# Performance work log

Measured on AMD Instinct MI355X. Metric: run time of the kernel, lower is better.

The kernel has to match this reference:

```python
import jax, jax.numpy as jnp
import numpy as np

N_, CIN, H_, W_ = 2, 128, 240, 320
C_, HEADS, WS, DEPTH, HID, DOUT, NQ = 128, 4, 7, 4, 512, 256, 128

def _ln(x, g, b, eps=1e-5):
    mu = x.mean(-1, keepdims=True)
    var = ((x - mu) ** 2).mean(-1, keepdims=True)
    return (x - mu) / jnp.sqrt(var + eps) * g + b

def setup_inputs() -> dict:
    key = jax.random.key(0)
    ks = jax.random.split(key, 16)
    s = 0.02
    d = {}
    d['x'] = jax.random.normal(ks[0], (N_, CIN, H_, W_), jnp.float32)
    d['conv_w'] = jax.random.normal(ks[1], (C_, CIN), jnp.float32) * s
    d['conv_b'] = jnp.zeros((C_,), jnp.float32)
    d['n1_g'] = jnp.ones((DEPTH, C_), jnp.float32)
    d['n1_b'] = jnp.zeros((DEPTH, C_), jnp.float32)
    d['qkv_w'] = jax.random.normal(ks[2], (DEPTH, 3 * C_, C_), jnp.float32) * s
    d['qkv_b'] = jnp.zeros((DEPTH, 3 * C_), jnp.float32)
    d['proj_w'] = jax.random.normal(ks[3], (DEPTH, C_, C_), jnp.float32) * s
    d['proj_b'] = jnp.zeros((DEPTH, C_), jnp.float32)
    d['n2_g'] = jnp.ones((DEPTH, C_), jnp.float32)
    d['n2_b'] = jnp.zeros((DEPTH, C_), jnp.float32)
    d['fc1_w'] = jax.random.normal(ks[4], (DEPTH, HID, C_), jnp.float32) * s
    d['fc1_b'] = jnp.zeros((DEPTH, HID), jnp.float32)
    d['fc2_w'] = jax.random.normal(ks[5], (DEPTH, C_, HID), jnp.float32) * s
    d['fc2_b'] = jnp.zeros((DEPTH, C_), jnp.float32)
    d['r1_w'] = jax.random.normal(ks[6], (256, C_), jnp.float32) * s
    d['r1_b'] = jnp.zeros((256,), jnp.float32)
    d['r2_w'] = jax.random.normal(ks[7], (256, 256), jnp.float32) * s
    d['r2_b'] = jnp.zeros((256,), jnp.float32)
    d['r3_w'] = jax.random.normal(ks[8], (DOUT, 256), jnp.float32) * s
    d['r3_b'] = jnp.zeros((DOUT,), jnp.float32)
    return d

def _block(t, H, W, n1_g, n1_b, qkv_w, qkv_b, proj_w, proj_b, n2_g, n2_b, fc1_w, fc1_b, fc2_w, fc2_b):
    N, L, C = t.shape
    hd = C // HEADS
    scale = hd ** -0.5
    shortcut = t
    h = _ln(t, n1_g, n1_b).reshape(N, H, W, C)
    pad_h = (-H) % WS
    pad_w = (-W) % WS
    h = jnp.pad(h, ((0, 0), (0, pad_h), (0, pad_w), (0, 0)))
    Hp, Wp = H + pad_h, W + pad_w
    # partition into (num_windows*N, ws*ws, C)
    h = h.reshape(N, Hp // WS, WS, Wp // WS, WS, C).transpose(0, 1, 3, 2, 4, 5).reshape(-1, WS * WS, C)
    B_ = h.shape[0]
    qkv = (h @ qkv_w.T + qkv_b).reshape(B_, WS * WS, 3, HEADS, hd).transpose(2, 0, 3, 1, 4)
    q, k, v = qkv[0], qkv[1], qkv[2]
    attn = jax.nn.softmax(jnp.einsum('bhqd,bhkd->bhqk', q, k) * scale, axis=-1)
    o = jnp.einsum('bhqk,bhkd->bhqd', attn, v).transpose(0, 2, 1, 3).reshape(B_, WS * WS, C)
    o = o @ proj_w.T + proj_b
    # reverse window partition
    o = o.reshape(N, Hp // WS, Wp // WS, WS, WS, C).transpose(0, 1, 3, 2, 4, 5).reshape(N, Hp, Wp, C)[:, :H, :W, :].reshape(N, H * W, C)
    t = shortcut + o
    h2 = _ln(t, n2_g, n2_b)
    m = jax.nn.gelu(h2 @ fc1_w.T + fc1_b, approximate=False) @ fc2_w.T + fc2_b
    return t + m

def reference(x, conv_w, conv_b, n1_g, n1_b, qkv_w, qkv_b, proj_w, proj_b, n2_g, n2_b, fc1_w, fc1_b, fc2_w, fc2_b, r1_w, r1_b, r2_w, r2_b, r3_w, r3_b):
    N, Cin, H, W = x.shape
    xp = jnp.einsum('nchw,ec->nehw', x, conv_w) + conv_b[None, :, None, None]  # (N,C,H,W)
    tokens = xp.reshape(N, C_, H * W).transpose(0, 2, 1)  # (N,HW,C)
    for i in range(DEPTH):
        tokens = _block(tokens, H, W, n1_g[i], n1_b[i], qkv_w[i], qkv_b[i], proj_w[i], proj_b[i], n2_g[i], n2_b[i], fc1_w[i], fc1_b[i], fc2_w[i], fc2_b[i])
    head = tokens.mean(axis=1)  # (N,C)
    queries = tokens[:, :NQ, :]  # (N,NQ,C)
    maps = jnp.einsum('nchw,nqc->nqhw', xp, queries)  # PixelWiseDotProduct
    y = jax.nn.leaky_relu(head @ r1_w.T + r1_b, 0.01)
    y = jax.nn.leaky_relu(y @ r2_w.T + r2_b, 0.01)
    y = y @ r3_w.T + r3_b
    y = jax.nn.relu(y) + 0.1  # norm == 'linear'
    y = y / y.sum(axis=1, keepdims=True)
    return (y, maps)
```

## Files before the change

kernel.cpp:

```cpp
#include <hip/hip_runtime.h>
#include <hip/hip_bf16.h>

typedef __hip_bfloat16 bf16;

static constexpr int Nn = 2, CIN = 128, Hh = 240, Ww = 320, HW = 76800;
static constexpr int Cc = 128, HID = 512, DOUT = 256, WSQ = 49;
static constexpr int NWH = 35, NWW = 46, WPN = NWH * NWW;
static constexpr int NWIN = Nn * WPN;
static constexpr float SCALE = 0.17677669529663687f;

typedef __attribute__((ext_vector_type(8))) short s8;
typedef __attribute__((ext_vector_type(4))) short s4;
typedef __attribute__((ext_vector_type(2))) short s2;
typedef __attribute__((ext_vector_type(4))) float f4;

__device__ __forceinline__ short f2bf(float x) {
  union { bf16 b; short s; } u; u.b = __float2bfloat16(x); return u.s;
}

#define MFMA(a, b, c) __builtin_amdgcn_mfma_f32_16x16x32_bf16((a), (b), (c), 0, 0, 0)

__global__ __launch_bounds__(256) void cast_bf16(const float* __restrict__ src,
                                                 short* __restrict__ dst, int n) {
  const int i = (blockIdx.x * 256 + threadIdx.x) * 4;
  if (i < n) {
    const float4 v = *(const float4*)(src + i);
    s4 o; o[0] = f2bf(v.x); o[1] = f2bf(v.y); o[2] = f2bf(v.z); o[3] = f2bf(v.w);
    *(s4*)(dst + i) = o;
  }
}

__global__ void init_head(float* headbuf) {
  if (threadIdx.x < 256) headbuf[threadIdx.x] = 0.f;
}

__global__ __launch_bounds__(256) void transp_w(const float* __restrict__ conv_w,
                                                float* __restrict__ wT) {
  const int idx = blockIdx.x * 256 + threadIdx.x;
  const int c = idx >> 7, e = idx & 127;
  wT[c * 128 + e] = conv_w[e * 128 + c];
}

__global__ __launch_bounds__(256) void conv_kernel(
    const float* __restrict__ x, const float* __restrict__ wT, const float* __restrict__ conv_b,
    float* __restrict__ tok) {
  __shared__ float wlds[64 * 128];
  const int tid = threadIdx.x;
  const int lane = tid & 63, w = tid >> 6;
  const int n = blockIdx.y;
  const int hw0 = blockIdx.x * 128;
  const int hwi = 2 * lane;
  const int e0 = 32 * w;
  const float* xn = x + (size_t)n * CIN * HW + hw0 + hwi;
  float acc[2][32];
#pragma unroll
  for (int jj = 0; jj < 8; jj++) {
    const float4 b4 = *(const float4*)(conv_b + e0 + jj * 4);
    acc[0][jj*4+0] = b4.x; acc[1][jj*4+0] = b4.x;
    acc[0][jj*4+1] = b4.y; acc[1][jj*4+1] = b4.y;
    acc[0][jj*4+2] = b4.z; acc[1][jj*4+2] = b4.z;
    acc[0][jj*4+3] = b4.w; acc[1][jj*4+3] = b4.w;
  }
  for (int ch = 0; ch < 2; ch++) {
    if (ch) __syncthreads();
    for (int idx = tid * 4; idx < 8192; idx += 1024)
      *(float4*)(wlds + idx) = *(const float4*)(wT + ch * 8192 + idx);
    __syncthreads();
    const float* xc = xn + (size_t)(64 * ch) * HW;
    float2 xv = *(const float2*)(xc);
    for (int cc = 0; cc < 64; cc++) {
      const float2 nxt = *(const float2*)(xc + (size_t)(cc < 63 ? cc + 1 : 63) * HW);
      const float* wl = wlds + cc * 128 + e0;
#pragma unroll
      for (int jj = 0; jj < 8; jj++) {
        const float4 w4 = *(const float4*)(wl + jj * 4);
        acc[0][jj*4+0] = fmaf(w4.x, xv.x, acc[0][jj*4+0]); acc[1][jj*4+0] = fmaf(w4.x, xv.y, acc[1][jj*4+0]);
        acc[0][jj*4+1] = fmaf(w4.y, xv.x, acc[0][jj*4+1]); acc[1][jj*4+1] = fmaf(w4.y, xv.y, acc[1][jj*4+1]);
        acc[0][jj*4+2] = fmaf(w4.z, xv.x, acc[0][jj*4+2]); acc[1][jj*4+2] = fmaf(w4.z, xv.y, acc[1][jj*4+2]);
        acc[0][jj*4+3] = fmaf(w4.w, xv.x, acc[0][jj*4+3]); acc[1][jj*4+3] = fmaf(w4.w, xv.y, acc[1][jj*4+3]);
      }
      xv = nxt;
    }
  }
  float* tb0 = tok + ((size_t)n * HW + hw0 + hwi) * Cc + e0;
  float* tb1 = tb0 + Cc;
#pragma unroll
  for (int jj = 0; jj < 8; jj++) {
    *(float4*)(tb0 + jj * 4) = make_float4(acc[0][jj*4], acc[0][jj*4+1], acc[0][jj*4+2], acc[0][jj*4+3]);
    *(float4*)(tb1 + jj * 4) = make_float4(acc[1][jj*4], acc[1][jj*4+1], acc[1][jj*4+2], acc[1][jj*4+3]);
  }
}

__global__ __launch_bounds__(256, 2) void attn_kernel(
    float* __restrict__ tok,
    const float* __restrict__ n1_g, const float* __restrict__ n1_b,
    const short* __restrict__ wqkv, const float* __restrict__ qkv_b,
    const short* __restrict__ wproj, const float* __restrict__ proj_b,
    int layer) {
  __shared__ __align__(16) short ms[27136];
  short* xwv = ms + 17920;

  const int tid = threadIdx.x;
  const int w = tid >> 6, lane = tid & 63;
  const int lq = lane >> 4, li = lane & 15;
  const int wi = blockIdx.x;
  const int n = wi / WPN;
  const int r0 = wi % WPN;
  const int wh = r0 / NWW, ww = r0 % NWW;

  const short* wqkv_l = wqkv + (size_t)layer * 384 * 128;
  const short* wproj_l = wproj + (size_t)layer * 128 * 128;

  for (int ti = w; ti < WSQ; ti += 4) {
    const int hh = wh * 7 + ti / 7, wv = ww * 7 + ti % 7;
    const bool valid = (hh < Hh) && (wv < Ww);
    float2 v = make_float2(0.f, 0.f);
    if (valid) v = *(const float2*)(tok + ((size_t)n * HW + hh * Ww + wv) * Cc + 2 * lane);
    float s = v.x + v.y, q = v.x * v.x + v.y * v.y;
#pragma unroll
    for (int m = 1; m < 64; m <<= 1) { s += __shfl_xor(s, m); q += __shfl_xor(q, m); }
    const float mean = s * (1.f / 128.f);
    const float rstd = rsqrtf(fmaxf(q * (1.f / 128.f) - mean * mean, 0.f) + 1e-5f);
    const int c = 2 * lane;
    float o0 = 0.f, o1 = 0.f;
    if (valid) {
      o0 = (v.x - mean) * rstd * n1_g[layer * Cc + c]     + n1_b[layer * Cc + c];
      o1 = (v.y - mean) * rstd * n1_g[layer * Cc + c + 1] + n1_b[layer * Cc + c + 1];
    }
    s2 pk; pk[0] = f2bf(o0); pk[1] = f2bf(o1);
    *(s2*)(xwv + ti * 136 + c) = pk;
  }
  for (int idx = tid; idx < 15 * 136; idx += 256) {
    xwv[(49 + idx / 136) * 136 + (idx % 136)] = 0;
  }
  __syncthreads();

  {
    const int n0 = 64 * w;
    f4 acc[4][4];
#pragma unroll
    for (int mt = 0; mt < 4; mt++)
#pragma unroll
      for (int nt = 0; nt < 4; nt++) acc[mt][nt] = f4{0.f, 0.f, 0.f, 0.f};
    for (int s = 0; s < 4; s++) {
      s8 a[4], b[4];
#pragma unroll
      for (int mt = 0; mt < 4; mt++)
        a[mt] = *(const s8*)(wqkv_l + (n0 + mt * 16 + li) * 128 + s * 32 + lq * 8);
#pragma unroll
      for (int nt = 0; nt < 4; nt++)
        b[nt] = *(const s8*)(xwv + (nt * 16 + li) * 136 + s * 32 + lq * 8);
#pragma unroll
      for (int mt = 0; mt < 4; mt++)
#pragma unroll
        for (int nt = 0; nt < 4; nt++) acc[mt][nt] = MFMA(a[mt], b[nt], acc[mt][nt]);
    }
    const bool isq = (w < 2);
    const float scl = isq ? SCALE : 1.f;
    const int koff = isq ? 0 : 2240;
#pragma unroll
    for (int mt = 0; mt < 4; mt++) {
      const int nbase = n0 + mt * 16 + lq * 4;
      const int hsel = (isq ? nbase : (nbase - 128)) >> 5;
      const int d0 = nbase & 31;
      const float4 bb = *(const float4*)(qkv_b + layer * 384 + nbase);
#pragma unroll
      for (int nt = 0; nt < 4; nt++) {
        const int tokn = nt * 16 + li;
        if (tokn < 56) {
          s4 pk;
          pk[0] = f2bf((acc[mt][nt][0] + bb.x) * scl);
          pk[1] = f2bf((acc[mt][nt][1] + bb.y) * scl);
          pk[2] = f2bf((acc[mt][nt][2] + bb.z) * scl);
          pk[3] = f2bf((acc[mt][nt][3] + bb.w) * scl);
          *(s4*)(ms + hsel * 4480 + koff + tokn * 40 + d0) = pk;
        }
      }
    }
  }

  {
    const int n0v = 32 * w;
    f4 acc2[4][2];
#pragma unroll
    for (int mt = 0; mt < 4; mt++)
#pragma unroll
      for (int nt = 0; nt < 2; nt++) acc2[mt][nt] = f4{0.f, 0.f, 0.f, 0.f};
    for (int s = 0; s < 4; s++) {
      s8 a[4], b[2];
#pragma unroll
      for (int mt = 0; mt < 4; mt++)
        a[mt] = *(const s8*)(xwv + (mt * 16 + li) * 136 + s * 32 + lq * 8);
#pragma unroll
      for (int nt = 0; nt < 2; nt++)
        b[nt] = *(const s8*)(wqkv_l + (256 + n0v + nt * 16 + li) * 128 + s * 32 + lq * 8);
#pragma unroll
      for (int mt = 0; mt < 4; mt++)
#pragma unroll
        for (int nt = 0; nt < 2; nt++) acc2[mt][nt] = MFMA(a[mt], b[nt], acc2[mt][nt]);
    }
    __syncthreads();
#pragma unroll
    for (int nt = 0; nt < 2; nt++) {
      const int d = n0v + nt * 16 + li;
      const float bv = qkv_b[layer * 384 + 256 + d];
#pragma unroll
      for (int mt = 0; mt < 4; mt++) {
        const int m0 = mt * 16 + lq * 4;
        s4 pk;
        pk[0] = f2bf(acc2[mt][nt][0] + bv);
        pk[1] = f2bf(acc2[mt][nt][1] + bv);
        pk[2] = f2bf(acc2[mt][nt][2] + bv);
        pk[3] = f2bf(acc2[mt][nt][3] + bv);
        *(s4*)(xwv + d * 72 + m0) = pk;
      }
    }
  }

  {
    short* qbase = ms + w * 4480;
    short* kbase = qbase + 2240;
    s8 ak[4], bq[4];
#pragma unroll
    for (int kt = 0; kt < 4; kt++) ak[kt] = *(const s8*)(kbase + (kt * 16 + li) * 40 + lq * 8);
#pragma unroll
    for (int qt = 0; qt < 4; qt++) bq[qt] = *(const s8*)(qbase + (qt * 16 + li) * 40 + lq * 8);
    f4 sc[4][4];
#pragma unroll
    for (int kt = 0; kt < 4; kt++)
#pragma unroll
      for (int qt = 0; qt < 4; qt++) sc[kt][qt] = f4{0.f, 0.f, 0.f, 0.f};
#pragma unroll
    for (int kt = 0; kt < 4; kt++)
#pragma unroll
      for (int qt = 0; qt < 4; qt++) sc[kt][qt] = MFMA(ak[kt], bq[qt], sc[kt][qt]);
#pragma unroll
    for (int kt = 0; kt < 4; kt++)
#pragma unroll
      for (int r = 0; r < 4; r++)
        if (kt * 16 + lq * 4 + r >= WSQ) {
#pragma unroll
          for (int qt = 0; qt < 4; qt++) sc[kt][qt][r] = -1e30f;
        }
    float inv[4];
#pragma unroll
    for (int qt = 0; qt < 4; qt++) {
      float m = -1e30f;
#pragma unroll
      for (int kt = 0; kt < 4; kt++)
#pragma unroll
        for (int r = 0; r < 4; r++) m = fmaxf(m, sc[kt][qt][r]);
      m = fmaxf(m, __shfl_xor(m, 16));
      m = fmaxf(m, __shfl_xor(m, 32));
      float ssum = 0.f;
#pragma unroll
      for (int kt = 0; kt < 4; kt++)
#pragma unroll
        for (int r = 0; r < 4; r++) {
          const float e = __expf(sc[kt][qt][r] - m);
          sc[kt][qt][r] = e; ssum += e;
        }
      ssum += __shfl_xor(ssum, 16);
      ssum += __shfl_xor(ssum, 32);
      inv[qt] = 1.f / ssum;
    }
#pragma unroll
    for (int qt = 0; qt < 4; qt++) {
      const int qq = qt * 16 + li;
      if (qq < 56) {
#pragma unroll
        for (int kt = 0; kt < 4; kt++) {
          s4 pk;
          pk[0] = f2bf(sc[kt][qt][0] * inv[qt]);
          pk[1] = f2bf(sc[kt][qt][1] * inv[qt]);
          pk[2] = f2bf(sc[kt][qt][2] * inv[qt]);
          pk[3] = f2bf(sc[kt][qt][3] * inv[qt]);
          *(s4*)(qbase + qq * 72 + kt * 16 + lq * 4) = pk;
        }
      }
    }
    f4 ov[2][4];
#pragma unroll
    for (int dt = 0; dt < 2; dt++)
#pragma unroll
      for (int qt = 0; qt < 4; qt++) ov[dt][qt] = f4{0.f, 0.f, 0.f, 0.f};
    for (int s = 0; s < 2; s++) {
      s8 av[2], bp[4];
#pragma unroll
      for (int dt = 0; dt < 2; dt++)
        av[dt] = *(const s8*)(xwv + (w * 32 + dt * 16 + li) * 72 + s * 32 + lq * 8);
#pragma unroll
      for (int qt = 0; qt < 4; qt++)
        bp[qt] = *(const s8*)(qbase + (qt * 16 + li) * 72 + s * 32 + lq * 8);
#pragma unroll
      for (int dt = 0; dt < 2; dt++)
#pragma unroll
        for (int qt = 0; qt < 4; qt++) ov[dt][qt] = MFMA(av[dt], bp[qt], ov[dt][qt]);
    }
    short* ohb = qbase;
#pragma unroll
    for (int dt = 0; dt < 2; dt++) {
      const int dl0 = dt * 16 + lq * 4;
#pragma unroll
      for (int qt = 0; qt < 4; qt++) {
        const int tokn = qt * 16 + li;
        s4 pk;
        pk[0] = f2bf(ov[dt][qt][0]);
        pk[1] = f2bf(ov[dt][qt][1]);
        pk[2] = f2bf(ov[dt][qt][2]);
        pk[3] = f2bf(ov[dt][qt][3]);
        *(s4*)(ohb + tokn * 40 + dl0) = pk;
      }
    }
  }
  __syncthreads();

  {
    const int n0p = 32 * w;
    f4 pa[4][2];
#pragma unroll
    for (int mt = 0; mt < 4; mt++)
#pragma unroll
      for (int nt = 0; nt < 2; nt++) pa[mt][nt] = f4{0.f, 0.f, 0.f, 0.f};
    for (int s = 0; s < 4; s++) {
      s8 ao[4], bw[2];
#pragma unroll
      for (int mt = 0; mt < 4; mt++)
        ao[mt] = *(const s8*)(ms + s * 4480 + (mt * 16 + li) * 40 + lq * 8);
#pragma unroll
      for (int nt = 0; nt < 2; nt++)
        bw[nt] = *(const s8*)(wproj_l + (n0p + nt * 16 + li) * 128 + s * 32 + lq * 8);
#pragma unroll
      for (int mt = 0; mt < 4; mt++)
#pragma unroll
        for (int nt = 0; nt < 2; nt++) pa[mt][nt] = MFMA(ao[mt], bw[nt], pa[mt][nt]);
    }
#pragma unroll
    for (int nt = 0; nt < 2; nt++) {
      const int c = n0p + nt * 16 + li;
      const float pb = proj_b[layer * 128 + c];
#pragma unroll
      for (int mt = 0; mt < 4; mt++) {
#pragma unroll
        for (int r = 0; r < 4; r++) {
          const int m = mt * 16 + lq * 4 + r;
          if (m < WSQ) {
            const int hh = wh * 7 + m / 7, wv = ww * 7 + m % 7;
            if (hh < Hh && wv < Ww) {
              float* p = tok + ((size_t)n * HW + hh * Ww + wv) * Cc + c;
              *p += pa[mt][nt][r] + pb;
            }
          }
        }
      }
    }
  }
}

__global__ __launch_bounds__(256, 3) void mlp_kernel(
    float* __restrict__ tok,
    const float* __restrict__ n2_g, const float* __restrict__ n2_b,
    const short* __restrict__ wfc1, const float* __restrict__ fc1_b,
    const short* __restrict__ wfc2, const float* __restrict__ fc2_b,
    int layer) {
  __shared__ __align__(16) short lnb[64 * 136];
  __shared__ __align__(16) short hbuf[2][64 * 136];

  const int tid = threadIdx.x;
  const int w = tid >> 6, lane = tid & 63;
  const int lq = lane >> 4, li = lane & 15;
  const int t0 = blockIdx.x * 64;
  const short* wfc1_l = wfc1 + (size_t)layer * 512 * 128;
  const short* wfc2_l = wfc2 + (size_t)layer * 128 * 512;

#pragma unroll
  for (int i = 0; i < 16; i++) {
    const int tl = w * 16 + i;
    const float2 v = *(const float2*)(tok + (size_t)(t0 + tl) * Cc + 2 * lane);
    float s = v.x + v.y, q = v.x * v.x + v.y * v.y;
#pragma unroll
    for (int m = 1; m < 64; m <<= 1) { s += __shfl_xor(s, m); q += __shfl_xor(q, m); }
    const float mean = s * (1.f / 128.f);
    const float rstd = rsqrtf(fmaxf(q * (1.f / 128.f) - mean * mean, 0.f) + 1e-5f);
    const int c = 2 * lane;
    s2 pk;
    pk[0] = f2bf((v.x - mean) * rstd * n2_g[layer * Cc + c]     + n2_b[layer * Cc + c]);
    pk[1] = f2bf((v.y - mean) * rstd * n2_g[layer * Cc + c + 1] + n2_b[layer * Cc + c + 1]);
    *(s2*)(lnb + tl * 136 + c) = pk;
  }
  __syncthreads();

  f4 acc2[2][4];
#pragma unroll
  for (int mt = 0; mt < 2; mt++)
#pragma unroll
    for (int nt = 0; nt < 4; nt++) acc2[mt][nt] = f4{0.f, 0.f, 0.f, 0.f};
  const int c0 = 32 * w;

  for (int s = 0; s < 4; s++) {
    f4 acc1[2][4];
#pragma unroll
    for (int mt = 0; mt < 2; mt++)
#pragma unroll
      for (int nt = 0; nt < 4; nt++) acc1[mt][nt] = f4{0.f, 0.f, 0.f, 0.f};
    const int hbase = 128 * s + 32 * w;
    for (int kc = 0; kc < 4; kc++) {
      s8 a[2], b[4];
#pragma unroll
      for (int mt = 0; mt < 2; mt++)
        a[mt] = *(const s8*)(wfc1_l + (hbase + mt * 16 + li) * 128 + kc * 32 + lq * 8);
#pragma unroll
      for (int nt = 0; nt < 4; nt++)
        b[nt] = *(const s8*)(lnb + (nt * 16 + li) * 136 + kc * 32 + lq * 8);
#pragma unroll
      for (int mt = 0; mt < 2; mt++)
#pragma unroll
        for (int nt = 0; nt < 4; nt++) acc1[mt][nt] = MFMA(a[mt], b[nt], acc1[mt][nt]);
    }
    short* hb = hbuf[s & 1];
#pragma unroll
    for (int mt = 0; mt < 2; mt++) {
      const int hl0 = 32 * w + mt * 16 + lq * 4;
      const float4 bb = *(const float4*)(fc1_b + layer * HID + 128 * s + hl0);
#pragma unroll
      for (int nt = 0; nt < 4; nt++) {
        const int tokn = nt * 16 + li;
        const float g0 = acc1[mt][nt][0] + bb.x, g1 = acc1[mt][nt][1] + bb.y;
        const float g2 = acc1[mt][nt][2] + bb.z, g3 = acc1[mt][nt][3] + bb.w;
        s4 pk;
        pk[0] = f2bf(0.5f * g0 * (1.f + erff(g0 * 0.70710678118654752f)));
        pk[1] = f2bf(0.5f * g1 * (1.f + erff(g1 * 0.70710678118654752f)));
        pk[2] = f2bf(0.5f * g2 * (1.f + erff(g2 * 0.70710678118654752f)));
        pk[3] = f2bf(0.5f * g3 * (1.f + erff(g3 * 0.70710678118654752f)));
        *(s4*)(hb + tokn * 136 + hl0) = pk;
      }
    }
    __syncthreads();
    for (int kc = 0; kc < 4; kc++) {
      s8 a[2], b[4];
#pragma unroll
      for (int mt = 0; mt < 2; mt++)
        a[mt] = *(const s8*)(wfc2_l + (c0 + mt * 16 + li) * 512 + s * 128 + kc * 32 + lq * 8);
#pragma unroll
      for (int nt = 0; nt < 4; nt++)
        b[nt] = *(const s8*)(hb + (nt * 16 + li) * 136 + kc * 32 + lq * 8);
#pragma unroll
      for (int mt = 0; mt < 2; mt++)
#pragma unroll
        for (int nt = 0; nt < 4; nt++) acc2[mt][nt] = MFMA(a[mt], b[nt], acc2[mt][nt]);
    }
  }

#pragma unroll
  for (int mt = 0; mt < 2; mt++) {
    const int cb = c0 + mt * 16 + lq * 4;
    const float4 bb = *(const float4*)(fc2_b + layer * Cc + cb);
#pragma unroll
    for (int nt = 0; nt < 4; nt++) {
      const int tokn = nt * 16 + li;
      float* p = tok + (size_t)(t0 + tokn) * Cc + cb;
      const float4 g = *(const float4*)p;
      *(float4*)p = make_float4(g.x + acc2[mt][nt][0] + bb.x,
                                g.y + acc2[mt][nt][1] + bb.y,
                                g.z + acc2[mt][nt][2] + bb.z,
                                g.w + acc2[mt][nt][3] + bb.w);
    }
  }
}

__global__ __launch_bounds__(256) void head_kernel(const float* __restrict__ tok,
                                                   float* __restrict__ headbuf) {
  const int n = blockIdx.x >> 6, slice = blockIdx.x & 63;
  const int c = threadIdx.x & 127, half = threadIdx.x >> 7;
  const float* base = tok + ((size_t)n * HW + slice * 1200 + half * 600) * Cc + c;
  float s = 0.f;
  for (int i = 0; i < 600; i++) s += base[(size_t)i * Cc];
  atomicAdd(&headbuf[n * 128 + c], s * (1.f / 76800.f));
}

__global__ __launch_bounds__(256) void y_kernel(
    const float* __restrict__ headbuf,
    const float* __restrict__ r1_w, const float* __restrict__ r1_b,
    const float* __restrict__ r2_w, const float* __restrict__ r2_b,
    const float* __restrict__ r3_w, const float* __restrict__ r3_b,
    float* __restrict__ yout) {
  __shared__ float hb[128], y1[256], y2[256], red4[4];
  const int tid = threadIdx.x;
  const int n = blockIdx.x;
  if (tid < 128) hb[tid] = headbuf[n * 128 + tid];
  __syncthreads();
  {
    float s = r1_b[tid];
    const float* w = r1_w + (size_t)tid * 128;
    for (int c = 0; c < 128; c += 4) {
      const float4 w4 = *(const float4*)(w + c);
      s = fmaf(w4.x, hb[c], s); s = fmaf(w4.y, hb[c+1], s);
      s = fmaf(w4.z, hb[c+2], s); s = fmaf(w4.w, hb[c+3], s);
    }
    y1[tid] = s >= 0.f ? s : 0.01f * s;
  }
  __syncthreads();
  {
    float s = r2_b[tid];
    const float* w = r2_w + (size_t)tid * 256;
    for (int c = 0; c < 256; c += 4) {
      const float4 w4 = *(const float4*)(w + c);
      s = fmaf(w4.x, y1[c], s); s = fmaf(w4.y, y1[c+1], s);
      s = fmaf(w4.z, y1[c+2], s); s = fmaf(w4.w, y1[c+3], s);
    }
    y2[tid] = s >= 0.f ? s : 0.01f * s;
  }
  __syncthreads();
  float v;
  {
    float s = r3_b[tid];
    const float* w = r3_w + (size_t)tid * 256;
    for (int c = 0; c < 256; c += 4) {
      const float4 w4 = *(const float4*)(w + c);
      s = fmaf(w4.x, y2[c], s); s = fmaf(w4.y, y2[c+1], s);
      s = fmaf(w4.z, y2[c+2], s); s = fmaf(w4.w, y2[c+3], s);
    }
    v = (s > 0.f ? s : 0.f) + 0.1f;
  }
  float t = v;
#pragma unroll
  for (int m = 1; m < 64; m <<= 1) t += __shfl_xor(t, m);
  if ((tid & 63) == 0) red4[tid >> 6] = t;
  __syncthreads();
  const float tot = red4[0] + red4[1] + red4[2] + red4[3];
  yout[n * DOUT + tid] = v / tot;
}

__global__ __launch_bounds__(256) void qprep_kernel(
    const float* __restrict__ tok, const float* __restrict__ conv_w, const float* __restrict__ conv_b,
    float* __restrict__ qwx, float* __restrict__ qb) {
  __shared__ float qs[16 * 128];
  const int tid = threadIdx.x;
  const int n = blockIdx.x >> 3, g = blockIdx.x & 7;
  const int q0 = g * 16;
  for (int idx = tid; idx < 2048; idx += 256)
    qs[idx] = tok[((size_t)n * HW + q0 + (idx >> 7)) * Cc + (idx & 127)];
  __syncthreads();
  const int c = tid & 127, half = tid >> 7;
  float acc[8];
#pragma unroll
  for (int j = 0; j < 8; j++) acc[j] = 0.f;
  for (int e = 0; e < 128; e += 4) {
    const float w0 = conv_w[(e + 0) * 128 + c];
    const float w1 = conv_w[(e + 1) * 128 + c];
    const float w2 = conv_w[(e + 2) * 128 + c];
    const float w3 = conv_w[(e + 3) * 128 + c];
#pragma unroll
    for (int j = 0; j < 8; j++) {
      const float4 qv = *(const float4*)(qs + (half * 8 + j) * 128 + e);
      acc[j] = fmaf(qv.x, w0, fmaf(qv.y, w1, fmaf(qv.z, w2, fmaf(qv.w, w3, acc[j]))));
    }
  }
  float* dst = qwx + ((size_t)n * 128 + c) * 128 + q0 + half * 8;
#pragma unroll
  for (int j = 0; j < 8; j++) dst[j] = acc[j];
  if (tid < 16) {
    float s = 0.f;
    for (int e = 0; e < 128; e += 4) {
      const float4 qv = *(const float4*)(qs + tid * 128 + e);
      const float4 bv = *(const float4*)(conv_b + e);
      s = fmaf(qv.x, bv.x, fmaf(qv.y, bv.y, fmaf(qv.z, bv.z, fmaf(qv.w, bv.w, s))));
    }
    qb[n * 128 + q0 + tid] = s;
  }
}

__global__ __launch_bounds__(256) void maps_kernel(
    const float* __restrict__ x, const float* __restrict__ qwx, const float* __restrict__ qb,
    float* __restrict__ mout) {
  __shared__ float qlds[64 * 128];
  const int tid = threadIdx.x;
  const int lane = tid & 63, w = tid >> 6;
  const int n = blockIdx.y;
  const int hw0 = blockIdx.x * 128;
  const int hwi = 2 * lane;
  const int q0 = 32 * w;
  const float* xn = x + (size_t)n * CIN * HW + hw0 + hwi;
  float acc[2][32];
#pragma unroll
  for (int jj = 0; jj < 8; jj++) {
    const float4 b4 = *(const float4*)(qb + n * 128 + q0 + jj * 4);
    acc[0][jj*4+0] = b4.x; acc[1][jj*4+0] = b4.x;
    acc[0][jj*4+1] = b4.y; acc[1][jj*4+1] = b4.y;
    acc[0][jj*4+2] = b4.z; acc[1][jj*4+2] = b4.z;
    acc[0][jj*4+3] = b4.w; acc[1][jj*4+3] = b4.w;
  }
  for (int ch = 0; ch < 2; ch++) {
    if (ch) __syncthreads();
    for (int idx = tid * 4; idx < 8192; idx += 1024)
      *(float4*)(qlds + idx) = *(const float4*)(qwx + (size_t)n * 16384 + ch * 8192 + idx);
    __syncthreads();
    const float* xc = xn + (size_t)(64 * ch) * HW;
    float2 xv = *(const float2*)(xc);
    for (int cc = 0; cc < 64; cc++) {
      const float2 nxt = *(const float2*)(xc + (size_t)(cc < 63 ? cc + 1 : 63) * HW);
      const float* ql = qlds + cc * 128 + q0;
#pragma unroll
      for (int jj = 0; jj < 8; jj++) {
        const float4 w4 = *(const float4*)(ql + jj * 4);
        acc[0][jj*4+0] = fmaf(w4.x, xv.x, acc[0][jj*4+0]); acc[1][jj*4+0] = fmaf(w4.x, xv.y, acc[1][jj*4+0]);
        acc[0][jj*4+1] = fmaf(w4.y, xv.x, acc[0][jj*4+1]); acc[1][jj*4+1] = fmaf(w4.y, xv.y, acc[1][jj*4+1]);
        acc[0][jj*4+2] = fmaf(w4.z, xv.x, acc[0][jj*4+2]); acc[1][jj*4+2] = fmaf(w4.z, xv.y, acc[1][jj*4+2]);
        acc[0][jj*4+3] = fmaf(w4.w, xv.x, acc[0][jj*4+3]); acc[1][jj*4+3] = fmaf(w4.w, xv.y, acc[1][jj*4+3]);
      }
      xv = nxt;
    }
  }
  float* mb = mout + ((size_t)n * 128 + q0) * HW + hw0 + hwi;
#pragma unroll
  for (int jj = 0; jj < 32; jj++) {
    *(float2*)(mb + (size_t)jj * HW) = make_float2(acc[0][jj], acc[1][jj]);
  }
}

extern "C" void kernel_launch(void* const* d_in, const int* in_sizes, int n_in,
                              void* d_out, int out_size, void* d_ws, size_t ws_size,
                              hipStream_t stream) {
  const float* x      = (const float*)d_in[0];
  const float* conv_w = (const float*)d_in[1];
  const float* conv_b = (const float*)d_in[2];
  const float* n1_g   = (const float*)d_in[3];
  const float* n1_b   = (const float*)d_in[4];
  const float* qkv_w  = (const float*)d_in[5];
  const float* qkv_b  = (const float*)d_in[6];
  const float* proj_w = (const float*)d_in[7];
  const float* proj_b = (const float*)d_in[8];
  const float* n2_g   = (const float*)d_in[9];
  const float* n2_b   = (const float*)d_in[10];
  const float* fc1_w  = (const float*)d_in[11];
  const float* fc1_b  = (const float*)d_in[12];
  const float* fc2_w  = (const float*)d_in[13];
  const float* fc2_b  = (const float*)d_in[14];
  const float* r1_w   = (const float*)d_in[15];
  const float* r1_b   = (const float*)d_in[16];
  const float* r2_w   = (const float*)d_in[17];
  const float* r2_b   = (const float*)d_in[18];
  const float* r3_w   = (const float*)d_in[19];
  const float* r3_b   = (const float*)d_in[20];

  float* out = (float*)d_out;
  float* tok = out + 512;

  char* ws = (char*)d_ws;
  short* wqkv = (short*)ws;
  short* wproj = (short*)(ws + 393216);
  short* wfc1 = (short*)(ws + 524288);
  short* wfc2 = (short*)(ws + 1048576);
  float* qwx = (float*)(ws + 1572864);
  float* qb = (float*)(ws + 1703936);
  float* headbuf = (float*)(ws + 1704960);
  float* wconvT = qwx;

  cast_bf16<<<196608 / 1024, 256, 0, stream>>>(qkv_w, wqkv, 196608);
  cast_bf16<<<65536 / 1024, 256, 0, stream>>>(proj_w, wproj, 65536);
  cast_bf16<<<262144 / 1024, 256, 0, stream>>>(fc1_w, wfc1, 262144);
  cast_bf16<<<262144 / 1024, 256, 0, stream>>>(fc2_w, wfc2, 262144);
  init_head<<<1, 256, 0, stream>>>(headbuf);
  transp_w<<<64, 256, 0, stream>>>(conv_w, wconvT);
  conv_kernel<<<dim3(600, 2), 256, 0, stream>>>(x, wconvT, conv_b, tok);
  for (int l = 0; l < 4; l++) {
    attn_kernel<<<NWIN, 256, 0, stream>>>(tok, n1_g, n1_b, wqkv, qkv_b, wproj, proj_b, l);
    mlp_kernel<<<2400, 256, 0, stream>>>(tok, n2_g, n2_b, wfc1, fc1_b, wfc2, fc2_b, l);
  }
  head_kernel<<<128, 256, 0, stream>>>(tok, headbuf);
  y_kernel<<<2, 256, 0, stream>>>(headbuf, r1_w, r1_b, r2_w, r2_b, r3_w, r3_b, out);
  qprep_kernel<<<16, 256, 0, stream>>>(tok, conv_w, conv_b, qwx, qb);
  maps_kernel<<<dim3(600, 2), 256, 0, stream>>>(x, qwx, qb, out + 512);
}
```

Measured before the change: 1.542 ms.

## Stage window tokens through LDS with float4 loads and coalesced residual writeback

The attention kernel now loads each window's fp32 tokens into shared memory with coalesced float4 loads before layernorm, instead of per-wave float2 loads. The output projection result is written to an LDS tile and then added to the residual with vectorized float4 read-modify-write, replacing scattered scalar updates. The per-head Q/K slices are trimmed from 56 to 52 rows to shrink the LDS footprint, which may allow more resident blocks. The cost is extra syncthreads and LDS traffic, and the LDS regions are reused between stages.

Measured after the change: 1.339 ms. -13.1%, faster.

```diff
diff --git a/kernel.cpp b/kernel.cpp
--- a/kernel.cpp
+++ b/kernel.cpp
@@ -8,6 +8,11 @@
 static constexpr int NWH = 35, NWW = 46, WPN = NWH * NWW;
 static constexpr int NWIN = Nn * WPN;
 static constexpr float SCALE = 0.17677669529663687f;
+
+static constexpr int SLICE = 4160;
+static constexpr int KOFF  = 2080;
+static constexpr int TRIM  = 52;
+static constexpr int XWOFF = 16640;
 
 typedef __attribute__((ext_vector_type(8))) short s8;
 typedef __attribute__((ext_vector_type(4))) short s4;
@@ -97,8 +102,8 @@
     const short* __restrict__ wqkv, const float* __restrict__ qkv_b,
     const short* __restrict__ wproj, const float* __restrict__ proj_b,
     int layer) {
-  __shared__ __align__(16) short ms[27136];
-  short* xwv = ms + 17920;
+  __shared__ __align__(16) short ms[25856];
+  short* xwv = ms + XWOFF;
 
   const int tid = threadIdx.x;
   const int w = tid >> 6, lane = tid & 63;
@@ -111,27 +116,37 @@
   const short* wqkv_l = wqkv + (size_t)layer * 384 * 128;
   const short* wproj_l = wproj + (size_t)layer * 128 * 128;
 
-  for (int ti = w; ti < WSQ; ti += 4) {
-    const int hh = wh * 7 + ti / 7, wv = ww * 7 + ti % 7;
-    const bool valid = (hh < Hh) && (wv < Ww);
-    float2 v = make_float2(0.f, 0.f);
-    if (valid) v = *(const float2*)(tok + ((size_t)n * HW + hh * Ww + wv) * Cc + 2 * lane);
-    float s = v.x + v.y, q = v.x * v.x + v.y * v.y;
-#pragma unroll
-    for (int m = 1; m < 64; m <<= 1) { s += __shfl_xor(s, m); q += __shfl_xor(q, m); }
-    const float mean = s * (1.f / 128.f);
-    const float rstd = rsqrtf(fmaxf(q * (1.f / 128.f) - mean * mean, 0.f) + 1e-5f);
-    const int c = 2 * lane;
-    float o0 = 0.f, o1 = 0.f;
-    if (valid) {
-      o0 = (v.x - mean) * rstd * n1_g[layer * Cc + c]     + n1_b[layer * Cc + c];
-      o1 = (v.y - mean) * rstd * n1_g[layer * Cc + c + 1] + n1_b[layer * Cc + c + 1];
-    }
-    s2 pk; pk[0] = f2bf(o0); pk[1] = f2bf(o1);
-    *(s2*)(xwv + ti * 136 + c) = pk;
-  }
-  for (int idx = tid; idx < 15 * 136; idx += 256) {
-    xwv[(49 + idx / 136) * 136 + (idx % 136)] = 0;
+  {
+    float* g32 = (float*)ms;
+    for (int idx = tid; idx < WSQ * 32; idx += 256) {
+      const int t = idx >> 5, c4 = (idx & 31) * 4;
+      const int hh = wh * 7 + t / 7, wv = ww * 7 + t % 7;
+      float4 v = make_float4(0.f, 0.f, 0.f, 0.f);
+      if (hh < Hh && wv < Ww)
+        v = *(const float4*)(tok + ((size_t)n * HW + hh * Ww + wv) * Cc + c4);
+      *(float4*)(g32 + t * 128 + c4) = v;
+    }
+    for (int idx = tid; idx < 15 * 136; idx += 256)
+      xwv[(49 + idx / 136) * 136 + (idx % 136)] = 0;
+    __syncthreads();
+    for (int ti = w; ti < WSQ; ti += 4) {
+      const int hh = wh * 7 + ti / 7, wv = ww * 7 + ti % 7;
+      const bool valid = (hh < Hh) && (wv < Ww);
+      const float2 v = *(const float2*)(g32 + ti * 128 + 2 * lane);
+      float s = v.x + v.y, q = v.x * v.x + v.y * v.y;
+#pragma unroll
+      for (int m = 1; m < 64; m <<= 1) { s += __shfl_xor(s, m); q += __shfl_xor(q, m); }
+      const float mean = s * (1.f / 128.f);
+      const float rstd = rsqrtf(fmaxf(q * (1.f / 128.f) - mean * mean, 0.f) + 1e-5f);
+      const int c = 2 * lane;
+      float o0 = 0.f, o1 = 0.f;
+      if (valid) {
+        o0 = (v.x - mean) * rstd * n1_g[layer * Cc + c]     + n1_b[layer * Cc + c];
+        o1 = (v.y - mean) * rstd * n1_g[layer * Cc + c + 1] + n1_b[layer * Cc + c + 1];
+      }
+      s2 pk; pk[0] = f2bf(o0); pk[1] = f2bf(o1);
+      *(s2*)(xwv + ti * 136 + c) = pk;
+    }
   }
   __syncthreads();
 
@@ -157,7 +172,7 @@
     }
     const bool isq = (w < 2);
     const float scl = isq ? SCALE : 1.f;
-    const int koff = isq ? 0 : 2240;
+    const int koff = isq ? 0 : KOFF;
 #pragma unroll
     for (int mt = 0; mt < 4; mt++) {
       const int nbase = n0 + mt * 16 + lq * 4;
@@ -167,13 +182,13 @@
 #pragma unroll
       for (int nt = 0; nt < 4; nt++) {
         const int tokn = nt * 16 + li;
-        if (tokn < 56) {
+        if (tokn < TRIM) {
           s4 pk;
           pk[0] = f2bf((acc[mt][nt][0] + bb.x) * scl);
           pk[1] = f2bf((acc[mt][nt][1] + bb.y) * scl);
           pk[2] = f2bf((acc[mt][nt][2] + bb.z) * scl);
           pk[3] = f2bf((acc[mt][nt][3] + bb.w) * scl);
-          *(s4*)(ms + hsel * 4480 + koff + tokn * 40 + d0) = pk;
+          *(s4*)(ms + hsel * SLICE + koff + tokn * 40 + d0) = pk;
         }
       }
     }
@@ -218,8 +233,8 @@
   }
 
   {
-    short* qbase = ms + w * 4480;
-    short* kbase = qbase + 2240;
+    short* qbase = ms + w * SLICE;
+    short* kbase = qbase + KOFF;
     s8 ak[4], bq[4];
 #pragma unroll
     for (int kt = 0; kt < 4; kt++) ak[kt] = *(const s8*)(kbase + (kt * 16 + li) * 40 + lq * 8);
@@ -267,7 +282,7 @@
 #pragma unroll
     for (int qt = 0; qt < 4; qt++) {
       const int qq = qt * 16 + li;
-      if (qq < 56) {
+      if (qq < TRIM) {
 #pragma unroll
         for (int kt = 0; kt < 4; kt++) {
           s4 pk;
@@ -326,7 +341,7 @@
       s8 ao[4], bw[2];
 #pragma unroll
       for (int mt = 0; mt < 4; mt++)
-        ao[mt] = *(const s8*)(ms + s * 4480 + (mt * 16 + li) * 40 + lq * 8);
+        ao[mt] = *(const s8*)(ms + s * SLICE + (mt * 16 + li) * 40 + lq * 8);
 #pragma unroll
       for (int nt = 0; nt < 2; nt++)
         bw[nt] = *(const s8*)(wproj_l + (n0p + nt * 16 + li) * 128 + s * 32 + lq * 8);
@@ -335,23 +350,31 @@
 #pragma unroll
         for (int nt = 0; nt < 2; nt++) pa[mt][nt] = MFMA(ao[mt], bw[nt], pa[mt][nt]);
     }
+    __syncthreads();
+    float* res = (float*)ms;
 #pragma unroll
     for (int nt = 0; nt < 2; nt++) {
       const int c = n0p + nt * 16 + li;
-      const float pb = proj_b[layer * 128 + c];
 #pragma unroll
       for (int mt = 0; mt < 4; mt++) {
 #pragma unroll
         for (int r = 0; r < 4; r++) {
           const int m = mt * 16 + lq * 4 + r;
-          if (m < WSQ) {
-            const int hh = wh * 7 + m / 7, wv = ww * 7 + m % 7;
-            if (hh < Hh && wv < Ww) {
-              float* p = tok + ((size_t)n * HW + hh * Ww + wv) * Cc + c;
-              *p += pa[mt][nt][r] + pb;
-            }
-          }
+          res[m * 132 + c] = pa[mt][nt][r];
         }
+      }
+    }
+    __syncthreads();
+    for (int idx = tid; idx < WSQ * 32; idx += 256) {
+      const int t = idx >> 5, c4 = (idx & 31) * 4;
+      const int hh = wh * 7 + t / 7, wv = ww * 7 + t % 7;
+      if (hh < Hh && wv < Ww) {
+        float* p = tok + ((size_t)n * HW + hh * Ww + wv) * Cc + c4;
+        const float4 g = *(const float4*)p;
+        const float4 r4 = *(const float4*)(res + t * 132 + c4);
+        const float4 pb4 = *(const float4*)(proj_b + layer * 128 + c4);
+        *(float4*)p = make_float4(g.x + r4.x + pb4.x, g.y + r4.y + pb4.y,
+                                  g.z + r4.z + pb4.z, g.w + r4.w + pb4.w);
       }
     }
   }
```
